# Optimization experiments

Measured on AMD Instinct MI355X. Metric: run time of the kernel, lower is better.

Reference implementation:

```python
import jax, jax.numpy as jnp
import numpy as np

T = 4096        # tokens
D = 1024        # input_dim
H = 2048        # expert_hidden_dim
O = 1024        # output_dim
E = 8           # num_experts
K = 2           # top_k


def setup_inputs() -> dict:
    key = jax.random.key(0)
    ks = jax.random.split(key, 7)
    s_in = 1.0 / np.sqrt(D)
    s_h = 1.0 / np.sqrt(H)
    return {
        "x": jax.random.normal(ks[0], (T, D), dtype=jnp.float32),
        "Wg": jax.random.uniform(ks[1], (D, E), jnp.float32, -s_in, s_in),
        "bg": jax.random.uniform(ks[2], (E,), jnp.float32, -s_in, s_in),
        "W1": jax.random.uniform(ks[3], (E, D, H), jnp.float32, -s_in, s_in),
        "b1": jax.random.uniform(ks[4], (E, H), jnp.float32, -s_in, s_in),
        "W2": jax.random.uniform(ks[5], (E, H, O), jnp.float32, -s_h, s_h),
        "b2": jax.random.uniform(ks[6], (E, O), jnp.float32, -s_h, s_h),
    }


def reference(x, Wg, bg, W1, b1, W2, b2):
    # Gating: top-k over expert logits, softmax over the k selected logits.
    logits = x @ Wg + bg                                  # [T, E]
    top_vals, top_idx = jax.lax.top_k(logits, K)          # [T, K]
    gates = jax.nn.softmax(top_vals, axis=-1)             # [T, K]

    # Expert MLPs (Linear -> ReLU -> Linear). Each token is processed by the
    # experts it routes to; since an expert's output on x is route-independent,
    # compute all expert outputs once and gather the selected ones (static
    # shapes, jit-friendly equivalent of the masked dispatch loop).
    h = jax.nn.relu(jnp.einsum('td,edh->eth', x, W1) + b1[:, None, :])  # [E,T,H]
    y = jnp.einsum('eth,eho->eto', h, W2) + b2[:, None, :]              # [E,T,O]

    sel = y[top_idx, jnp.arange(T)[:, None]]              # [T, K, O]
    # Weighted combine (scatter_add over batch_idx == per-token sum over K).
    return jnp.sum(sel * gates[..., None], axis=1)        # [T, O]
```

## Files before the change

### kernel.cpp

```cpp
#include <hip/hip_runtime.h>
#include <math.h>


#define T_TOK 4096
#define DIM   1024
#define HID   2048
#define OUTD  1024
#define NE    8

typedef __bf16 bf16_t;
typedef __bf16 bf16x8 __attribute__((ext_vector_type(8)));
typedef float  f32x4  __attribute__((ext_vector_type(4)));

typedef __attribute__((address_space(3))) void       as3_void;
typedef __attribute__((address_space(1))) const void as1_void;
#define GLDS16(src, dst) \
  __builtin_amdgcn_global_load_lds((as1_void*)(src), (as3_void*)(dst), 16, 0, 0)

#define FENCE() asm volatile("" ::: "memory")
#define BARRIER() do { FENCE(); __builtin_amdgcn_s_barrier(); FENCE(); } while (0)

__global__ void k_gate(const float* __restrict__ x, const float* __restrict__ Wg,
                       const float* __restrict__ bg, int* __restrict__ einfo,
                       float2* __restrict__ gpair, bf16_t* __restrict__ xb) {
  int wid  = threadIdx.x >> 6;
  int lane = threadIdx.x & 63;
  int t = blockIdx.x * 4 + wid;

  const float4* xr = (const float4*)(x + (size_t)t * DIM);
  float4 xv4[4];
  float sf[NE];
#pragma unroll
  for (int e = 0; e < NE; ++e) sf[e] = 0.f;

#pragma unroll
  for (int i = 0; i < 4; ++i) {
    int q = lane + 64 * i;
    float4 xv = xr[q];
    xv4[i] = xv;
    int d = q * 4;
#pragma unroll
    for (int c = 0; c < 4; ++c) {
      float xc = (&xv.x)[c];
      const float4* wr = (const float4*)(Wg + (size_t)(d + c) * NE);
      float4 w0 = wr[0], w1 = wr[1];
      sf[0] += xc * w0.x; sf[1] += xc * w0.y;
      sf[2] += xc * w0.z; sf[3] += xc * w0.w;
      sf[4] += xc * w1.x; sf[5] += xc * w1.y;
      sf[6] += xc * w1.z; sf[7] += xc * w1.w;
    }
  }

  ushort4* xbr = (ushort4*)(xb + (size_t)t * DIM);
#pragma unroll
  for (int i = 0; i < 4; ++i) {
    union { bf16_t b[4]; ushort4 u; } cv;
    cv.b[0] = (bf16_t)xv4[i].x; cv.b[1] = (bf16_t)xv4[i].y;
    cv.b[2] = (bf16_t)xv4[i].z; cv.b[3] = (bf16_t)xv4[i].w;
    xbr[lane + 64 * i] = cv.u;
  }

  double s[NE];
#pragma unroll
  for (int e = 0; e < NE; ++e) s[e] = (double)sf[e];
#pragma unroll
  for (int off = 32; off > 0; off >>= 1) {
#pragma unroll
    for (int e = 0; e < NE; ++e) s[e] += __shfl_xor(s[e], off);
  }

  if (lane == 0) {
    double v0 = -1e300, v1 = -1e300;
    int i0 = 0, i1 = 0;
#pragma unroll
    for (int e = 0; e < NE; ++e) {
      double v = s[e] + (double)bg[e];
      if (v > v0)      { v1 = v0; i1 = i0; v0 = v; i0 = e; }
      else if (v > v1) { v1 = v;  i1 = e; }
    }
    float ex = expf((float)(v1 - v0));
    float inv = 1.0f / (1.0f + ex);
    einfo[t] = i0 | (i1 << 8);
    gpair[t] = make_float2(inv, ex * inv);
  }
}

__global__ void k_bin(const int* __restrict__ einfo, const float2* __restrict__ gpair,
                      int* __restrict__ cnt, int* __restrict__ offs,
                      int* __restrict__ elist, float* __restrict__ egate,
                      int* __restrict__ tokrec) {
  __shared__ int scnt[NE];
  int w = threadIdx.x >> 6;
  int lane = threadIdx.x & 63;
  unsigned long long below = (lane == 0) ? 0ull : ((~0ull) >> (64 - lane));
  int base = 0;
  for (int c = 0; c < T_TOK / 64; ++c) {
    int t = c * 64 + lane;
    int ei = einfo[t];
    float2 g = gpair[t];
    int e0 = ei & 0xff, e1 = ei >> 8;
    bool m0 = (e0 == w);
    bool m  = m0 || (e1 == w);
    unsigned long long mask = __ballot(m);
    if (m) {
      int pos = base + (int)__popcll(mask & below);
      elist[w * T_TOK + pos] = t;
      egate[w * T_TOK + pos] = m0 ? g.x : g.y;
      tokrec[2 * t + (m0 ? 0 : 1)] = (w << 16) | pos;
    }
    base += (int)__popcll(mask);
  }
  if (lane == 0) scnt[w] = base;
  __syncthreads();
  if (threadIdx.x == 0) {
    int a = 0;
#pragma unroll
    for (int e = 0; e < NE; ++e) {
      cnt[e] = scnt[e];
      offs[e] = a;
      a += scnt[e];
    }
    offs[NE] = a;
  }
}

__global__ void k_tr(const float* __restrict__ W, bf16_t* __restrict__ Wt,
                     int R, int C) {
  __shared__ float tile[32][33];
  size_t ebase = (size_t)blockIdx.z * R * C;
  int c0 = blockIdx.x * 32, r0 = blockIdx.y * 32;
  int id = threadIdx.x;
  int rc = id >> 5, cc = id & 31;
#pragma unroll
  for (int i = 0; i < 4; ++i)
    tile[rc + i * 8][cc] = W[ebase + (size_t)(r0 + rc + i * 8) * C + c0 + cc];
  __syncthreads();
  int oc = id >> 4, orp = id & 15;
  ushort2* wt2 = (ushort2*)(Wt + ebase);
#pragma unroll
  for (int i = 0; i < 2; ++i) {
    int c = oc + i * 16;
    union { bf16_t b[2]; ushort2 u; } cv;
    cv.b[0] = (bf16_t)tile[orp * 2][c];
    cv.b[1] = (bf16_t)tile[orp * 2 + 1][c];
    wt2[((size_t)(c0 + c) * R + r0 + orp * 2) >> 1] = cv.u;
  }
}


#define STAGE_A(TT, HH) do { \
    char* _d = smem + ((((TT) & 1) * 2 + (HH)) << 14); \
    GLDS16(Abase + offA[HH][0] + (TT) * 128, _d + dstq0 * 16); \
    GLDS16(Abase + offA[HH][1] + (TT) * 128, _d + dstq1 * 16); } while (0)

#define STAGE_B(TT, HH) do { \
    char* _d = smem + 65536 + ((((TT) & 1) * 2 + (HH)) << 14); \
    GLDS16(Bbase + offB[HH][0] + (TT) * 128, _d + dstq0 * 16); \
    GLDS16(Bbase + offB[HH][1] + (TT) * 128, _d + dstq1 * 16); } while (0)

#define MFMA_Q(AF, BF, AH, BH) \
    _Pragma("unroll") for (int i = 0; i < 4; ++i) \
      _Pragma("unroll") for (int j = 0; j < 2; ++j) \
        _Pragma("unroll") for (int kk = 0; kk < 2; ++kk) \
          acc[(AH) * 4 + i][(BH) * 2 + j] = \
            __builtin_amdgcn_mfma_f32_16x16x32_bf16(AF[i][kk], BF[j][kk], \
                acc[(AH) * 4 + i][(BH) * 2 + j], 0, 0, 0)

#define LGKM_WAIT() do { \
    asm volatile("s_waitcnt lgkmcnt(0)" ::: "memory"); \
    __builtin_amdgcn_sched_barrier(0); } while (0)

#define KTILE(TT, NTc) do { \
    const char* _a0 = smem + ((((TT) & 1) * 2 + 0) << 14); \
    const char* _a1 = smem + ((((TT) & 1) * 2 + 1) << 14); \
    const char* _b0 = smem + 65536 + ((((TT) & 1) * 2 + 0) << 14); \
    const char* _b1 = smem + 65536 + ((((TT) & 1) * 2 + 1) << 14); \
    bf16x8 af[4][2], bf0[2][2], bf1[2][2]; \
     \
    _Pragma("unroll") for (int i = 0; i < 4; ++i) \
      _Pragma("unroll") for (int kk = 0; kk < 2; ++kk) \
        af[i][kk] = *(const bf16x8*)(_a0 + rdA[i][kk]); \
    _Pragma("unroll") for (int j = 0; j < 2; ++j) \
      _Pragma("unroll") for (int kk = 0; kk < 2; ++kk) { \
        bf0[j][kk] = *(const bf16x8*)(_b0 + rdB[j][kk]); \
        bf1[j][kk] = *(const bf16x8*)(_b1 + rdB[j][kk]); \
      } \
    if ((TT) + 1 < (NTc)) { STAGE_A((TT) + 1, 1); STAGE_B((TT) + 1, 1); } \
    BARRIER(); LGKM_WAIT(); \
    __builtin_amdgcn_s_setprio(1); \
    MFMA_Q(af, bf0, 0, 0); MFMA_Q(af, bf1, 0, 1); \
    __builtin_amdgcn_s_setprio(0); BARRIER(); \
     \
    _Pragma("unroll") for (int i = 0; i < 4; ++i) \
      _Pragma("unroll") for (int kk = 0; kk < 2; ++kk) \
        af[i][kk] = *(const bf16x8*)(_a1 + rdA[i][kk]); \
    if ((TT) + 2 < (NTc)) { STAGE_A((TT) + 2, 0); STAGE_B((TT) + 2, 0); \
      asm volatile("s_waitcnt vmcnt(4)" ::: "memory"); } \
    else { asm volatile("s_waitcnt vmcnt(0)" ::: "memory"); } \
    BARRIER(); LGKM_WAIT(); \
    __builtin_amdgcn_s_setprio(1); \
    MFMA_Q(af, bf0, 1, 0); MFMA_Q(af, bf1, 1, 1); \
    __builtin_amdgcn_s_setprio(0); BARRIER(); \
  } while (0)

__launch_bounds__(512, 2)
__global__ void k_gemm1(const bf16_t* __restrict__ xb, const bf16_t* __restrict__ W1t,
                        const float* __restrict__ b1, const int* __restrict__ cnt,
                        const int* __restrict__ offs, const int* __restrict__ elist,
                        bf16_t* __restrict__ hbuf) {
  const int e = blockIdx.z;
  const int count = cnt[e];
  const int rt = blockIdx.y;
  if (rt * 256 >= count) return;
  const int nt = blockIdx.x;

  __shared__ __align__(16) char smem[131072];

  const int tid = threadIdx.x, lane = tid & 63, wid = tid >> 6;
  const int wm = wid >> 2, wn = wid & 3;
  const int fr = lane & 15, lh = lane >> 4;

  unsigned offA[2][2], offB[2][2];
  const int dstq0 = tid, dstq1 = 512 + tid;
#pragma unroll
  for (int j = 0; j < 2; ++j) {
    int q = j * 512 + tid;
    int r = q >> 3, sfg = (q & 7) ^ (r & 7);
#pragma unroll
    for (int h = 0; h < 2; ++h) {
      int gr = rt * 256 + h * 128 + r;
      if (gr > count - 1) gr = count - 1;
      int tok = elist[e * T_TOK + gr];
      offA[h][j] = (unsigned)((tok * DIM + sfg * 8) * 2);
      int brow = nt * 256 + h * 128 + r;
      offB[h][j] = (unsigned)(((e * HID + brow) * DIM + sfg * 8) * 2);
    }
  }
  unsigned rdA[4][2], rdB[2][2];
#pragma unroll
  for (int i = 0; i < 4; ++i) {
    int r = wm * 64 + i * 16 + fr;
#pragma unroll
    for (int kk = 0; kk < 2; ++kk)
      rdA[i][kk] = (unsigned)(r * 128 + (((kk * 4 + lh) ^ (r & 7)) * 16));
  }
#pragma unroll
  for (int j = 0; j < 2; ++j) {
    int r = wn * 32 + j * 16 + fr;
#pragma unroll
    for (int kk = 0; kk < 2; ++kk)
      rdB[j][kk] = (unsigned)(r * 128 + (((kk * 4 + lh) ^ (r & 7)) * 16));
  }

  const char* Abase = (const char*)xb;
  const char* Bbase = (const char*)W1t;

  f32x4 acc[8][4];
#pragma unroll
  for (int i = 0; i < 8; ++i)
#pragma unroll
    for (int j = 0; j < 4; ++j) acc[i][j] = (f32x4){0.f, 0.f, 0.f, 0.f};

  const int NT = DIM / 64;
  STAGE_A(0, 0); STAGE_B(0, 0); STAGE_A(0, 1); STAGE_B(0, 1);
  STAGE_A(1, 0); STAGE_B(1, 0);
  asm volatile("s_waitcnt vmcnt(4)" ::: "memory");
  BARRIER();

  for (int t = 0; t < NT; ++t) KTILE(t, NT);

  const int hbase = offs[e];
#pragma unroll
  for (int mi = 0; mi < 8; ++mi) {
#pragma unroll
    for (int rr = 0; rr < 4; ++rr) {
      int rowp = rt * 256 + (mi >> 2) * 128 + wm * 64 + (mi & 3) * 16 + lh * 4 + rr;
      if (rowp < count) {
        size_t hrow = (size_t)(hbase + rowp) * HID;
#pragma unroll
        for (int nj = 0; nj < 4; ++nj) {
          int col = nt * 256 + (nj >> 1) * 128 + wn * 32 + (nj & 1) * 16 + fr;
          float v = acc[mi][nj][rr] + b1[e * HID + col];
          hbuf[hrow + col] = (bf16_t)(v > 0.f ? v : 0.f);
        }
      }
    }
  }
}

__launch_bounds__(512, 2)
__global__ void k_gemm2(const bf16_t* __restrict__ hbuf, const bf16_t* __restrict__ W2t,
                        const float* __restrict__ b2, const int* __restrict__ cnt,
                        const int* __restrict__ offs, const float* __restrict__ egate,
                        float* __restrict__ y) {
  const int e = blockIdx.z;
  const int count = cnt[e];
  const int rt = blockIdx.y;
  if (rt * 256 >= count) return;
  const int nt = blockIdx.x;

  __shared__ __align__(16) char smem[131072];

  const int tid = threadIdx.x, lane = tid & 63, wid = tid >> 6;
  const int wm = wid >> 2, wn = wid & 3;
  const int fr = lane & 15, lh = lane >> 4;
  const int hbase = offs[e];

  unsigned offA[2][2], offB[2][2];
  const int dstq0 = tid, dstq1 = 512 + tid;
#pragma unroll
  for (int j = 0; j < 2; ++j) {
    int q = j * 512 + tid;
    int r = q >> 3, sfg = (q & 7) ^ (r & 7);
#pragma unroll
    for (int h = 0; h < 2; ++h) {
      int gr = rt * 256 + h * 128 + r;
      if (gr > count - 1) gr = count - 1;
      offA[h][j] = (unsigned)(((hbase + gr) * HID + sfg * 8) * 2);
      int brow = nt * 256 + h * 128 + r;
      offB[h][j] = (unsigned)(((e * OUTD + brow) * HID + sfg * 8) * 2);
    }
  }
  unsigned rdA[4][2], rdB[2][2];
#pragma unroll
  for (int i = 0; i < 4; ++i) {
    int r = wm * 64 + i * 16 + fr;
#pragma unroll
    for (int kk = 0; kk < 2; ++kk)
      rdA[i][kk] = (unsigned)(r * 128 + (((kk * 4 + lh) ^ (r & 7)) * 16));
  }
#pragma unroll
  for (int j = 0; j < 2; ++j) {
    int r = wn * 32 + j * 16 + fr;
#pragma unroll
    for (int kk = 0; kk < 2; ++kk)
      rdB[j][kk] = (unsigned)(r * 128 + (((kk * 4 + lh) ^ (r & 7)) * 16));
  }

  const char* Abase = (const char*)hbuf;
  const char* Bbase = (const char*)W2t;

  f32x4 acc[8][4];
#pragma unroll
  for (int i = 0; i < 8; ++i)
#pragma unroll
    for (int j = 0; j < 4; ++j) acc[i][j] = (f32x4){0.f, 0.f, 0.f, 0.f};

  const int NT = HID / 64;
  STAGE_A(0, 0); STAGE_B(0, 0); STAGE_A(0, 1); STAGE_B(0, 1);
  STAGE_A(1, 0); STAGE_B(1, 0);
  asm volatile("s_waitcnt vmcnt(4)" ::: "memory");
  BARRIER();

  for (int t = 0; t < NT; ++t) KTILE(t, NT);

#pragma unroll
  for (int mi = 0; mi < 8; ++mi) {
#pragma unroll
    for (int rr = 0; rr < 4; ++rr) {
      int rowp = rt * 256 + (mi >> 2) * 128 + wm * 64 + (mi & 3) * 16 + lh * 4 + rr;
      if (rowp < count) {
        float gate = egate[e * T_TOK + rowp];
        size_t yrow = (size_t)(hbase + rowp) * OUTD;
#pragma unroll
        for (int nj = 0; nj < 4; ++nj) {
          int col = nt * 256 + (nj >> 1) * 128 + wn * 32 + (nj & 1) * 16 + fr;
          y[yrow + col] = gate * (acc[mi][nj][rr] + b2[e * OUTD + col]);
        }
      }
    }
  }
}

__global__ void k_combine(const float* __restrict__ y, const int* __restrict__ offs,
                          const int* __restrict__ tokrec, float* __restrict__ out) {
  int t = blockIdx.x;
  int r0 = tokrec[2 * t], r1 = tokrec[2 * t + 1];
  int s0 = offs[r0 >> 16] + (r0 & 0xffff);
  int s1 = offs[r1 >> 16] + (r1 & 0xffff);
  const float4* ya = (const float4*)(y + (size_t)s0 * OUTD);
  const float4* yb = (const float4*)(y + (size_t)s1 * OUTD);
  float4* o = (float4*)(out + (size_t)t * OUTD);
  int i = threadIdx.x;
  float4 a = ya[i], b = yb[i];
  o[i] = make_float4(a.x + b.x, a.y + b.y, a.z + b.z, a.w + b.w);
}

extern "C" void kernel_launch(void* const* d_in, const int* in_sizes, int n_in,
                              void* d_out, int out_size, void* d_ws, size_t ws_size,
                              hipStream_t stream) {
  const float* x  = (const float*)d_in[0];
  const float* Wg = (const float*)d_in[1];
  const float* bg = (const float*)d_in[2];
  const float* W1 = (const float*)d_in[3];
  const float* b1 = (const float*)d_in[4];
  const float* W2 = (const float*)d_in[5];
  const float* b2 = (const float*)d_in[6];
  float* out = (float*)d_out;

  char* ws = (char*)d_ws;
  int*    cnt    = (int*)(ws);
  int*    offs   = (int*)(ws + 1024);
  int*    tokrec = (int*)(ws + 4096);
  int*    einfo  = (int*)(ws + 36864);
  float2* gpair  = (float2*)(ws + 53248);
  int*    elist  = (int*)(ws + 131072);
  float*  egate  = (float*)(ws + 262144);
  bf16_t* W1t    = (bf16_t*)(ws + (1u << 20));
  float*  y      = (float*)(ws + (1u << 20));
  bf16_t* W2t    = (bf16_t*)(ws + (1u << 20) + (32u << 20));
  bf16_t* xb     = (bf16_t*)(ws + (1u << 20) + (64u << 20));
  bf16_t* hbuf   = (bf16_t*)(ws + (1u << 20) + (72u << 20));

  k_gate<<<T_TOK / 4, 256, 0, stream>>>(x, Wg, bg, einfo, gpair, xb);
  k_bin<<<1, 512, 0, stream>>>(einfo, gpair, cnt, offs, elist, egate, tokrec);
  k_tr<<<dim3(HID / 32, DIM / 32, NE), 256, 0, stream>>>(W1, W1t, DIM, HID);
  k_tr<<<dim3(OUTD / 32, HID / 32, NE), 256, 0, stream>>>(W2, W2t, HID, OUTD);

  k_gemm1<<<dim3(HID / 256, 16, NE), 512, 0, stream>>>(
      xb, W1t, b1, cnt, offs, elist, hbuf);
  k_gemm2<<<dim3(OUTD / 256, 16, NE), 512, 0, stream>>>(
      hbuf, W2t, b2, cnt, offs, egate, y);
  k_combine<<<T_TOK, 256, 0, stream>>>(y, offs, tokrec, out);
}
```

Baseline: 232.4 us.

## Flatten grouped GEMM grid over concatenated expert rows and narrow gemm2 N-tile

Replaces the per-expert 3D grid (which launched mostly empty blocks and padded partial tiles) with a flat grid over the concatenated routed-row space, so each 256-row tile loops over the experts whose segments it overlaps. Tiles that only cover one 128-row half use a dedicated half-tile loop. k_bin now writes a flattened token list for gemm1. gemm2 also shrinks its N tile to 128 to double the block count and cut LDS use to 96KB. In exchange, tiles straddling an expert boundary are computed twice, and the half-tile path synchronises fully on every k-step.

```diff
diff --git a/kernel.cpp b/kernel.cpp
--- a/kernel.cpp
+++ b/kernel.cpp
@@ -19,6 +19,10 @@
 
 #define FENCE() asm volatile("" ::: "memory")
 #define BARRIER() do { FENCE(); __builtin_amdgcn_s_barrier(); FENCE(); } while (0)
+#define LGKM_WAIT() do { \
+    asm volatile("s_waitcnt lgkmcnt(0)" ::: "memory"); \
+    __builtin_amdgcn_sched_barrier(0); } while (0)
+#define VM_WAIT0() asm volatile("s_waitcnt vmcnt(0)" ::: "memory")
 
 __global__ void k_gate(const float* __restrict__ x, const float* __restrict__ Wg,
                        const float* __restrict__ bg, int* __restrict__ einfo,
@@ -88,7 +92,7 @@
 __global__ void k_bin(const int* __restrict__ einfo, const float2* __restrict__ gpair,
                       int* __restrict__ cnt, int* __restrict__ offs,
                       int* __restrict__ elist, float* __restrict__ egate,
-                      int* __restrict__ tokrec) {
+                      int* __restrict__ tokrec, int* __restrict__ ftok) {
   __shared__ int scnt[NE];
   int w = threadIdx.x >> 6;
   int lane = threadIdx.x & 63;
@@ -122,6 +126,13 @@
     }
     offs[NE] = a;
   }
+  int off_w = 0;
+#pragma unroll
+  for (int i = 0; i < NE; ++i)
+    if (i < w) off_w += scnt[i];
+  int n_w = scnt[w];
+  for (int p = lane; p < n_w; p += 64)
+    ftok[off_w + p] = elist[w * T_TOK + p];
 }
 
 __global__ void k_tr(const float* __restrict__ W, bf16_t* __restrict__ Wt,
@@ -147,18 +158,17 @@
   }
 }
 
-
-#define STAGE_A(TT, HH) do { \
+#define STAGE_A1(TT, HH) do { \
     char* _d = smem + ((((TT) & 1) * 2 + (HH)) << 14); \
     GLDS16(Abase + offA[HH][0] + (TT) * 128, _d + dstq0 * 16); \
     GLDS16(Abase + offA[HH][1] + (TT) * 128, _d + dstq1 * 16); } while (0)
 
-#define STAGE_B(TT, HH) do { \
+#define STAGE_B1(TT, HH) do { \
     char* _d = smem + 65536 + ((((TT) & 1) * 2 + (HH)) << 14); \
     GLDS16(Bbase + offB[HH][0] + (TT) * 128, _d + dstq0 * 16); \
     GLDS16(Bbase + offB[HH][1] + (TT) * 128, _d + dstq1 * 16); } while (0)
 
-#define MFMA_Q(AF, BF, AH, BH) \
+#define MFMA_Q1(AF, BF, AH, BH) \
     _Pragma("unroll") for (int i = 0; i < 4; ++i) \
       _Pragma("unroll") for (int j = 0; j < 2; ++j) \
         _Pragma("unroll") for (int kk = 0; kk < 2; ++kk) \
@@ -166,76 +176,90 @@
             __builtin_amdgcn_mfma_f32_16x16x32_bf16(AF[i][kk], BF[j][kk], \
                 acc[(AH) * 4 + i][(BH) * 2 + j], 0, 0, 0)
 
-#define LGKM_WAIT() do { \
-    asm volatile("s_waitcnt lgkmcnt(0)" ::: "memory"); \
-    __builtin_amdgcn_sched_barrier(0); } while (0)
-
-#define KTILE(TT, NTc) do { \
+#define RD_AF1(SL) \
+    _Pragma("unroll") for (int i = 0; i < 4; ++i) \
+      _Pragma("unroll") for (int kk = 0; kk < 2; ++kk) \
+        af[i][kk] = *(const bf16x8*)((SL) + rdA[i][kk])
+
+#define KTILE1(TT, NTc) do { \
     const char* _a0 = smem + ((((TT) & 1) * 2 + 0) << 14); \
     const char* _a1 = smem + ((((TT) & 1) * 2 + 1) << 14); \
     const char* _b0 = smem + 65536 + ((((TT) & 1) * 2 + 0) << 14); \
     const char* _b1 = smem + 65536 + ((((TT) & 1) * 2 + 1) << 14); \
     bf16x8 af[4][2], bf0[2][2], bf1[2][2]; \
-     \
-    _Pragma("unroll") for (int i = 0; i < 4; ++i) \
-      _Pragma("unroll") for (int kk = 0; kk < 2; ++kk) \
-        af[i][kk] = *(const bf16x8*)(_a0 + rdA[i][kk]); \
+    RD_AF1(_a0); \
     _Pragma("unroll") for (int j = 0; j < 2; ++j) \
       _Pragma("unroll") for (int kk = 0; kk < 2; ++kk) { \
         bf0[j][kk] = *(const bf16x8*)(_b0 + rdB[j][kk]); \
         bf1[j][kk] = *(const bf16x8*)(_b1 + rdB[j][kk]); \
       } \
-    if ((TT) + 1 < (NTc)) { STAGE_A((TT) + 1, 1); STAGE_B((TT) + 1, 1); } \
+    if ((TT) + 1 < (NTc)) { STAGE_A1((TT) + 1, 1); STAGE_B1((TT) + 1, 1); } \
     BARRIER(); LGKM_WAIT(); \
     __builtin_amdgcn_s_setprio(1); \
-    MFMA_Q(af, bf0, 0, 0); MFMA_Q(af, bf1, 0, 1); \
+    MFMA_Q1(af, bf0, 0, 0); MFMA_Q1(af, bf1, 0, 1); \
     __builtin_amdgcn_s_setprio(0); BARRIER(); \
-     \
-    _Pragma("unroll") for (int i = 0; i < 4; ++i) \
-      _Pragma("unroll") for (int kk = 0; kk < 2; ++kk) \
-        af[i][kk] = *(const bf16x8*)(_a1 + rdA[i][kk]); \
-    if ((TT) + 2 < (NTc)) { STAGE_A((TT) + 2, 0); STAGE_B((TT) + 2, 0); \
+    RD_AF1(_a1); \
+    if ((TT) + 2 < (NTc)) { STAGE_A1((TT) + 2, 0); STAGE_B1((TT) + 2, 0); \
       asm volatile("s_waitcnt vmcnt(4)" ::: "memory"); } \
-    else { asm volatile("s_waitcnt vmcnt(0)" ::: "memory"); } \
+    else { VM_WAIT0(); } \
     BARRIER(); LGKM_WAIT(); \
     __builtin_amdgcn_s_setprio(1); \
-    MFMA_Q(af, bf0, 1, 0); MFMA_Q(af, bf1, 1, 1); \
+    MFMA_Q1(af, bf0, 1, 0); MFMA_Q1(af, bf1, 1, 1); \
     __builtin_amdgcn_s_setprio(0); BARRIER(); \
   } while (0)
 
+#define G1_HALF(H) do { \
+    STAGE_A1(0, H); STAGE_B1(0, 0); STAGE_B1(0, 1); \
+    VM_WAIT0(); BARRIER(); \
+    for (int t = 0; t < NT; ++t) { \
+      const char* _a  = smem + (((t & 1) * 2 + (H)) << 14); \
+      const char* _b0 = smem + 65536 + (((t & 1) * 2 + 0) << 14); \
+      const char* _b1 = smem + 65536 + (((t & 1) * 2 + 1) << 14); \
+      bf16x8 af[4][2], bf0[2][2], bf1[2][2]; \
+      RD_AF1(_a); \
+      _Pragma("unroll") for (int j = 0; j < 2; ++j) \
+        _Pragma("unroll") for (int kk = 0; kk < 2; ++kk) { \
+          bf0[j][kk] = *(const bf16x8*)(_b0 + rdB[j][kk]); \
+          bf1[j][kk] = *(const bf16x8*)(_b1 + rdB[j][kk]); \
+        } \
+      if (t + 1 < NT) { STAGE_A1(t + 1, H); STAGE_B1(t + 1, 0); STAGE_B1(t + 1, 1); } \
+      LGKM_WAIT(); \
+      __builtin_amdgcn_s_setprio(1); \
+      MFMA_Q1(af, bf0, H, 0); MFMA_Q1(af, bf1, H, 1); \
+      __builtin_amdgcn_s_setprio(0); \
+      VM_WAIT0(); BARRIER(); \
+    } \
+  } while (0)
+
 __launch_bounds__(512, 2)
 __global__ void k_gemm1(const bf16_t* __restrict__ xb, const bf16_t* __restrict__ W1t,
-                        const float* __restrict__ b1, const int* __restrict__ cnt,
-                        const int* __restrict__ offs, const int* __restrict__ elist,
-                        bf16_t* __restrict__ hbuf) {
-  const int e = blockIdx.z;
-  const int count = cnt[e];
-  const int rt = blockIdx.y;
-  if (rt * 256 >= count) return;
-  const int nt = blockIdx.x;
+                        const float* __restrict__ b1, const int* __restrict__ offs,
+                        const int* __restrict__ ftok, bf16_t* __restrict__ hbuf) {
+  const int bid = blockIdx.x;
+  const int nt = bid & 7, rt = bid >> 3;
+  const int r0 = rt * 256;
 
   __shared__ __align__(16) char smem[131072];
 
   const int tid = threadIdx.x, lane = tid & 63, wid = tid >> 6;
   const int wm = wid >> 2, wn = wid & 3;
   const int fr = lane & 15, lh = lane >> 4;
-
-  unsigned offA[2][2], offB[2][2];
   const int dstq0 = tid, dstq1 = 512 + tid;
+
+  int rowq[2], sfgq[2];
 #pragma unroll
   for (int j = 0; j < 2; ++j) {
     int q = j * 512 + tid;
-    int r = q >> 3, sfg = (q & 7) ^ (r & 7);
-#pragma unroll
-    for (int h = 0; h < 2; ++h) {
-      int gr = rt * 256 + h * 128 + r;
-      if (gr > count - 1) gr = count - 1;
-      int tok = elist[e * T_TOK + gr];
-      offA[h][j] = (unsigned)((tok * DIM + sfg * 8) * 2);
-      int brow = nt * 256 + h * 128 + r;
-      offB[h][j] = (unsigned)(((e * HID + brow) * DIM + sfg * 8) * 2);
-    }
-  }
+    rowq[j] = q >> 3;
+    sfgq[j] = (q & 7) ^ (rowq[j] & 7);
+  }
+  unsigned offA[2][2];
+#pragma unroll
+  for (int j = 0; j < 2; ++j)
+#pragma unroll
+    for (int h = 0; h < 2; ++h)
+      offA[h][j] = (unsigned)((ftok[r0 + h * 128 + rowq[j]] * DIM + sfgq[j] * 8) * 2);
+
   unsigned rdA[4][2], rdB[2][2];
 #pragma unroll
   for (int i = 0; i < 4; ++i) {
@@ -254,74 +278,165 @@
 
   const char* Abase = (const char*)xb;
   const char* Bbase = (const char*)W1t;
-
-  f32x4 acc[8][4];
-#pragma unroll
-  for (int i = 0; i < 8; ++i)
-#pragma unroll
-    for (int j = 0; j < 4; ++j) acc[i][j] = (f32x4){0.f, 0.f, 0.f, 0.f};
-
   const int NT = DIM / 64;
-  STAGE_A(0, 0); STAGE_B(0, 0); STAGE_A(0, 1); STAGE_B(0, 1);
-  STAGE_A(1, 0); STAGE_B(1, 0);
-  asm volatile("s_waitcnt vmcnt(4)" ::: "memory");
-  BARRIER();
-
-  for (int t = 0; t < NT; ++t) KTILE(t, NT);
-
-  const int hbase = offs[e];
-#pragma unroll
-  for (int mi = 0; mi < 8; ++mi) {
-#pragma unroll
-    for (int rr = 0; rr < 4; ++rr) {
-      int rowp = rt * 256 + (mi >> 2) * 128 + wm * 64 + (mi & 3) * 16 + lh * 4 + rr;
-      if (rowp < count) {
-        size_t hrow = (size_t)(hbase + rowp) * HID;
-#pragma unroll
-        for (int nj = 0; nj < 4; ++nj) {
-          int col = nt * 256 + (nj >> 1) * 128 + wn * 32 + (nj & 1) * 16 + fr;
-          float v = acc[mi][nj][rr] + b1[e * HID + col];
-          hbuf[hrow + col] = (bf16_t)(v > 0.f ? v : 0.f);
+
+  int e = 0;
+  while (offs[e + 1] <= r0) ++e;
+  for (;;) {
+    const int lo = offs[e] > r0 ? offs[e] : r0;
+    const int hi = offs[e + 1] < r0 + 256 ? offs[e + 1] : r0 + 256;
+    if (hi > lo) {
+      unsigned offB[2][2];
+#pragma unroll
+      for (int j = 0; j < 2; ++j)
+#pragma unroll
+        for (int h = 0; h < 2; ++h)
+          offB[h][j] = (unsigned)(((e * HID + nt * 256 + h * 128 + rowq[j]) * DIM +
+                                   sfgq[j] * 8) * 2);
+
+      f32x4 acc[8][4];
+#pragma unroll
+      for (int i = 0; i < 8; ++i)
+#pragma unroll
+        for (int j = 0; j < 4; ++j) acc[i][j] = (f32x4){0.f, 0.f, 0.f, 0.f};
+
+      const bool fh0 = lo < r0 + 128, fh1 = hi > r0 + 128;
+      if (fh0 && fh1) {
+        STAGE_A1(0, 0); STAGE_B1(0, 0); STAGE_A1(0, 1); STAGE_B1(0, 1);
+        STAGE_A1(1, 0); STAGE_B1(1, 0);
+        asm volatile("s_waitcnt vmcnt(4)" ::: "memory");
+        BARRIER();
+        for (int t = 0; t < NT; ++t) KTILE1(t, NT);
+      } else if (fh0) {
+        G1_HALF(0);
+      } else {
+        G1_HALF(1);
+      }
+
+#pragma unroll
+      for (int mi = 0; mi < 8; ++mi) {
+#pragma unroll
+        for (int rr = 0; rr < 4; ++rr) {
+          int row = r0 + (mi >> 2) * 128 + wm * 64 + (mi & 3) * 16 + lh * 4 + rr;
+          if (row >= lo && row < hi) {
+            size_t hrow = (size_t)row * HID;
+#pragma unroll
+            for (int nj = 0; nj < 4; ++nj) {
+              int col = nt * 256 + (nj >> 1) * 128 + wn * 32 + (nj & 1) * 16 + fr;
+              float v = acc[mi][nj][rr] + b1[e * HID + col];
+              hbuf[hrow + col] = (bf16_t)(v > 0.f ? v : 0.f);
+            }
+          }
         }
       }
     }
-  }
-}
+    if (offs[e + 1] >= r0 + 256) break;
+    ++e;
+  }
+}
+
+#define STAGE_A2(TT, HH) do { \
+    char* _d = smem + ((((TT) & 1) * 2 + (HH)) << 14); \
+    GLDS16(Abase + offA[HH][0] + (TT) * 128, _d + dstq0 * 16); \
+    GLDS16(Abase + offA[HH][1] + (TT) * 128, _d + dstq1 * 16); } while (0)
+
+#define STAGE_B2(TT, HH) do { \
+    char* _d = smem + 65536 + ((((TT) & 1) * 2 + (HH)) << 13); \
+    GLDS16(Bbase + offB2[HH] + (TT) * 128, _d + tid * 16); } while (0)
+
+#define MFMA_Q2(AF, BF, AH, BH) \
+    _Pragma("unroll") for (int i = 0; i < 4; ++i) \
+      _Pragma("unroll") for (int kk = 0; kk < 2; ++kk) \
+        acc[(AH) * 4 + i][BH] = \
+          __builtin_amdgcn_mfma_f32_16x16x32_bf16(AF[i][kk], BF[kk], \
+              acc[(AH) * 4 + i][BH], 0, 0, 0)
+
+#define RD_AF2(SL) \
+    _Pragma("unroll") for (int i = 0; i < 4; ++i) \
+      _Pragma("unroll") for (int kk = 0; kk < 2; ++kk) \
+        af[i][kk] = *(const bf16x8*)((SL) + rdA[i][kk])
+
+#define KTILE2(TT, NTc) do { \
+    const char* _a0 = smem + ((((TT) & 1) * 2 + 0) << 14); \
+    const char* _a1 = smem + ((((TT) & 1) * 2 + 1) << 14); \
+    const char* _b0 = smem + 65536 + ((((TT) & 1) * 2 + 0) << 13); \
+    const char* _b1 = smem + 65536 + ((((TT) & 1) * 2 + 1) << 13); \
+    bf16x8 af[4][2], bf0[2], bf1[2]; \
+    RD_AF2(_a0); \
+    _Pragma("unroll") for (int kk = 0; kk < 2; ++kk) { \
+      bf0[kk] = *(const bf16x8*)(_b0 + rdB2[kk]); \
+      bf1[kk] = *(const bf16x8*)(_b1 + rdB2[kk]); \
+    } \
+    if ((TT) + 1 < (NTc)) { STAGE_A2((TT) + 1, 1); STAGE_B2((TT) + 1, 1); } \
+    BARRIER(); LGKM_WAIT(); \
+    __builtin_amdgcn_s_setprio(1); \
+    MFMA_Q2(af, bf0, 0, 0); MFMA_Q2(af, bf1, 0, 1); \
+    __builtin_amdgcn_s_setprio(0); BARRIER(); \
+    RD_AF2(_a1); \
+    if ((TT) + 2 < (NTc)) { STAGE_A2((TT) + 2, 0); STAGE_B2((TT) + 2, 0); \
+      asm volatile("s_waitcnt vmcnt(3)" ::: "memory"); } \
+    else { VM_WAIT0(); } \
+    BARRIER(); LGKM_WAIT(); \
+    __builtin_amdgcn_s_setprio(1); \
+    MFMA_Q2(af, bf0, 1, 0); MFMA_Q2(af, bf1, 1, 1); \
+    __builtin_amdgcn_s_setprio(0); BARRIER(); \
+  } while (0)
+
+#define G2_HALF(H) do { \
+    STAGE_A2(0, H); STAGE_B2(0, 0); STAGE_B2(0, 1); \
+    VM_WAIT0(); BARRIER(); \
+    for (int t = 0; t < NT; ++t) { \
+      const char* _a  = smem + (((t & 1) * 2 + (H)) << 14); \
+      const char* _b0 = smem + 65536 + (((t & 1) * 2 + 0) << 13); \
+      const char* _b1 = smem + 65536 + (((t & 1) * 2 + 1) << 13); \
+      bf16x8 af[4][2], bf0[2], bf1[2]; \
+      RD_AF2(_a); \
+      _Pragma("unroll") for (int kk = 0; kk < 2; ++kk) { \
+        bf0[kk] = *(const bf16x8*)(_b0 + rdB2[kk]); \
+        bf1[kk] = *(const bf16x8*)(_b1 + rdB2[kk]); \
+      } \
+      if (t + 1 < NT) { STAGE_A2(t + 1, H); STAGE_B2(t + 1, 0); STAGE_B2(t + 1, 1); } \
+      LGKM_WAIT(); \
+      __builtin_amdgcn_s_setprio(1); \
+      MFMA_Q2(af, bf0, H, 0); MFMA_Q2(af, bf1, H, 1); \
+      __builtin_amdgcn_s_setprio(0); \
+      VM_WAIT0(); BARRIER(); \
+    } \
+  } while (0)
 
 __launch_bounds__(512, 2)
 __global__ void k_gemm2(const bf16_t* __restrict__ hbuf, const bf16_t* __restrict__ W2t,
-                        const float* __restrict__ b2, const int* __restrict__ cnt,
-                        const int* __restrict__ offs, const float* __restrict__ egate,
-                        float* __restrict__ y) {
-  const int e = blockIdx.z;
-  const int count = cnt[e];
-  const int rt = blockIdx.y;
-  if (rt * 256 >= count) return;
-  const int nt = blockIdx.x;
-
-  __shared__ __align__(16) char smem[131072];
+                        const float* __restrict__ b2, const int* __restrict__ offs,
+                        const float* __restrict__ egate, float* __restrict__ y) {
+  const int bid = blockIdx.x;
+  const int nt = bid & 7, rt = bid >> 3;
+  const int r0 = rt * 256;
+
+  __shared__ __align__(16) char smem[98304];
 
   const int tid = threadIdx.x, lane = tid & 63, wid = tid >> 6;
   const int wm = wid >> 2, wn = wid & 3;
   const int fr = lane & 15, lh = lane >> 4;
-  const int hbase = offs[e];
-
-  unsigned offA[2][2], offB[2][2];
   const int dstq0 = tid, dstq1 = 512 + tid;
+
+  int rowq[2], sfgq[2];
 #pragma unroll
   for (int j = 0; j < 2; ++j) {
     int q = j * 512 + tid;
-    int r = q >> 3, sfg = (q & 7) ^ (r & 7);
-#pragma unroll
-    for (int h = 0; h < 2; ++h) {
-      int gr = rt * 256 + h * 128 + r;
-      if (gr > count - 1) gr = count - 1;
-      offA[h][j] = (unsigned)(((hbase + gr) * HID + sfg * 8) * 2);
-      int brow = nt * 256 + h * 128 + r;
-      offB[h][j] = (unsigned)(((e * OUTD + brow) * HID + sfg * 8) * 2);
-    }
-  }
-  unsigned rdA[4][2], rdB[2][2];
+    rowq[j] = q >> 3;
+    sfgq[j] = (q & 7) ^ (rowq[j] & 7);
+  }
+  unsigned offA[2][2];
+#pragma unroll
+  for (int j = 0; j < 2; ++j)
+#pragma unroll
+    for (int h = 0; h < 2; ++h)
+      offA[h][j] = (unsigned)(((r0 + h * 128 + rowq[j]) * HID + sfgq[j] * 8) * 2);
+
+  const int rowB = tid >> 3;
+  const int sfgB = (tid & 7) ^ (rowB & 7);
+
+  unsigned rdA[4][2], rdB2[2];
 #pragma unroll
   for (int i = 0; i < 4; ++i) {
     int r = wm * 64 + i * 16 + fr;
@@ -329,46 +444,67 @@
     for (int kk = 0; kk < 2; ++kk)
       rdA[i][kk] = (unsigned)(r * 128 + (((kk * 4 + lh) ^ (r & 7)) * 16));
   }
-#pragma unroll
-  for (int j = 0; j < 2; ++j) {
-    int r = wn * 32 + j * 16 + fr;
+  {
+    int r = wn * 16 + fr;
 #pragma unroll
     for (int kk = 0; kk < 2; ++kk)
-      rdB[j][kk] = (unsigned)(r * 128 + (((kk * 4 + lh) ^ (r & 7)) * 16));
+      rdB2[kk] = (unsigned)(r * 128 + (((kk * 4 + lh) ^ (r & 7)) * 16));
   }
 
   const char* Abase = (const char*)hbuf;
   const char* Bbase = (const char*)W2t;
-
-  f32x4 acc[8][4];
-#pragma unroll
-  for (int i = 0; i < 8; ++i)
-#pragma unroll
-    for (int j = 0; j < 4; ++j) acc[i][j] = (f32x4){0.f, 0.f, 0.f, 0.f};
-
   const int NT = HID / 64;
-  STAGE_A(0, 0); STAGE_B(0, 0); STAGE_A(0, 1); STAGE_B(0, 1);
-  STAGE_A(1, 0); STAGE_B(1, 0);
-  asm volatile("s_waitcnt vmcnt(4)" ::: "memory");
-  BARRIER();
-
-  for (int t = 0; t < NT; ++t) KTILE(t, NT);
-
-#pragma unroll
-  for (int mi = 0; mi < 8; ++mi) {
-#pragma unroll
-    for (int rr = 0; rr < 4; ++rr) {
-      int rowp = rt * 256 + (mi >> 2) * 128 + wm * 64 + (mi & 3) * 16 + lh * 4 + rr;
-      if (rowp < count) {
-        float gate = egate[e * T_TOK + rowp];
-        size_t yrow = (size_t)(hbase + rowp) * OUTD;
-#pragma unroll
-        for (int nj = 0; nj < 4; ++nj) {
-          int col = nt * 256 + (nj >> 1) * 128 + wn * 32 + (nj & 1) * 16 + fr;
-          y[yrow + col] = gate * (acc[mi][nj][rr] + b2[e * OUTD + col]);
+
+  int e = 0;
+  while (offs[e + 1] <= r0) ++e;
+  for (;;) {
+    const int lo = offs[e] > r0 ? offs[e] : r0;
+    const int hi = offs[e + 1] < r0 + 256 ? offs[e + 1] : r0 + 256;
+    if (hi > lo) {
+      unsigned offB2[2];
+#pragma unroll
+      for (int h = 0; h < 2; ++h)
+        offB2[h] = (unsigned)(((e * OUTD + nt * 128 + h * 64 + rowB) * HID +
+                               sfgB * 8) * 2);
+
+      f32x4 acc[8][2];
+#pragma unroll
+      for (int i = 0; i < 8; ++i)
+#pragma unroll
+        for (int j = 0; j < 2; ++j) acc[i][j] = (f32x4){0.f, 0.f, 0.f, 0.f};
+
+      const bool fh0 = lo < r0 + 128, fh1 = hi > r0 + 128;
+      if (fh0 && fh1) {
+        STAGE_A2(0, 0); STAGE_B2(0, 0); STAGE_A2(0, 1); STAGE_B2(0, 1);
+        STAGE_A2(1, 0); STAGE_B2(1, 0);
+        asm volatile("s_waitcnt vmcnt(3)" ::: "memory");
+        BARRIER();
+        for (int t = 0; t < NT; ++t) KTILE2(t, NT);
+      } else if (fh0) {
+        G2_HALF(0);
+      } else {
+        G2_HALF(1);
+      }
+
+#pragma unroll
+      for (int mi = 0; mi < 8; ++mi) {
+#pragma unroll
+        for (int rr = 0; rr < 4; ++rr) {
+          int row = r0 + (mi >> 2) * 128 + wm * 64 + (mi & 3) * 16 + lh * 4 + rr;
+          if (row >= lo && row < hi) {
+            float gate = egate[e * T_TOK + row - offs[e]];
+            size_t yrow = (size_t)row * OUTD;
+#pragma unroll
+            for (int bh = 0; bh < 2; ++bh) {
+              int col = nt * 128 + bh * 64 + wn * 16 + fr;
+              y[yrow + col] = gate * (acc[mi][bh][rr] + b2[e * OUTD + col]);
+            }
+          }
         }
       }
     }
+    if (offs[e + 1] >= r0 + 256) break;
+    ++e;
   }
 }
 
@@ -406,6 +542,7 @@
   float2* gpair  = (float2*)(ws + 53248);
   int*    elist  = (int*)(ws + 131072);
   float*  egate  = (float*)(ws + 262144);
+  int*    ftok   = (int*)(ws + 393216);
   bf16_t* W1t    = (bf16_t*)(ws + (1u << 20));
   float*  y      = (float*)(ws + (1u << 20));
   bf16_t* W2t    = (bf16_t*)(ws + (1u << 20) + (32u << 20));
@@ -413,13 +550,13 @@
   bf16_t* hbuf   = (bf16_t*)(ws + (1u << 20) + (72u << 20));
 
   k_gate<<<T_TOK / 4, 256, 0, stream>>>(x, Wg, bg, einfo, gpair, xb);
-  k_bin<<<1, 512, 0, stream>>>(einfo, gpair, cnt, offs, elist, egate, tokrec);
+  k_bin<<<1, 512, 0, stream>>>(einfo, gpair, cnt, offs, elist, egate, tokrec, ftok);
   k_tr<<<dim3(HID / 32, DIM / 32, NE), 256, 0, stream>>>(W1, W1t, DIM, HID);
   k_tr<<<dim3(OUTD / 32, HID / 32, NE), 256, 0, stream>>>(W2, W2t, HID, OUTD);
 
-  k_gemm1<<<dim3(HID / 256, 16, NE), 512, 0, stream>>>(
-      xb, W1t, b1, cnt, offs, elist, hbuf);
-  k_gemm2<<<dim3(OUTD / 256, 16, NE), 512, 0, stream>>>(
-      hbuf, W2t, b2, cnt, offs, egate, y);
+  k_gemm1<<<(T_TOK * 2 / 256) * (HID / 256), 512, 0, stream>>>(
+      xb, W1t, b1, offs, ftok, hbuf);
+  k_gemm2<<<(T_TOK * 2 / 256) * (OUTD / 128), 512, 0, stream>>>(
+      hbuf, W2t, b2, offs, egate, y);
   k_combine<<<T_TOK, 256, 0, stream>>>(y, offs, tokrec, out);
 }
```

Measured after the change: 304.3 us. 31.0% more time.

## Shrink GEMM M-tile to 192 rows and vectorize weight transpose

Applied to the files above, without the earlier changes.

The expert GEMMs now use 192-row token tiles instead of 256. This changes the LDS staging layout, the per-wave accumulator count, and the per-wave vmcnt waits, since some waves issue fewer async loads. The grid grows to 22 row tiles. The goal is to cut padded-row waste on per-expert token counts and improve load balance, at the cost of less reuse of each B tile. The weight transpose kernel switches to 64x64 tiles with float4 loads and 16-byte bf16 stores to reduce memory transactions.

```diff
diff --git a/kernel.cpp b/kernel.cpp
--- a/kernel.cpp
+++ b/kernel.cpp
@@ -19,6 +19,13 @@
 
 #define FENCE() asm volatile("" ::: "memory")
 #define BARRIER() do { FENCE(); __builtin_amdgcn_s_barrier(); FENCE(); } while (0)
+#define LGKM_WAIT() do { \
+    asm volatile("s_waitcnt lgkmcnt(0)" ::: "memory"); \
+    __builtin_amdgcn_sched_barrier(0); } while (0)
+#define VMW_RING() do { \
+    if (wid < 4) asm volatile("s_waitcnt vmcnt(4)" ::: "memory"); \
+    else         asm volatile("s_waitcnt vmcnt(3)" ::: "memory"); } while (0)
+#define VM_WAIT0() asm volatile("s_waitcnt vmcnt(0)" ::: "memory")
 
 __global__ void k_gate(const float* __restrict__ x, const float* __restrict__ Wg,
                        const float* __restrict__ bg, int* __restrict__ einfo,
@@ -126,60 +133,61 @@
 
 __global__ void k_tr(const float* __restrict__ W, bf16_t* __restrict__ Wt,
                      int R, int C) {
-  __shared__ float tile[32][33];
+  __shared__ float tile[64][68];
   size_t ebase = (size_t)blockIdx.z * R * C;
-  int c0 = blockIdx.x * 32, r0 = blockIdx.y * 32;
-  int id = threadIdx.x;
-  int rc = id >> 5, cc = id & 31;
-#pragma unroll
-  for (int i = 0; i < 4; ++i)
-    tile[rc + i * 8][cc] = W[ebase + (size_t)(r0 + rc + i * 8) * C + c0 + cc];
+  int c0 = blockIdx.x * 64, r0 = blockIdx.y * 64;
+  int tid = threadIdx.x;
+  int ty = tid >> 4, tx = tid & 15;
+#pragma unroll
+  for (int i = 0; i < 4; ++i) {
+    int row = ty + i * 16;
+    float4 v = *(const float4*)&W[ebase + (size_t)(r0 + row) * C + c0 + tx * 4];
+    *(float4*)&tile[row][tx * 4] = v;
+  }
   __syncthreads();
-  int oc = id >> 4, orp = id & 15;
-  ushort2* wt2 = (ushort2*)(Wt + ebase);
-#pragma unroll
-  for (int i = 0; i < 2; ++i) {
-    int c = oc + i * 16;
-    union { bf16_t b[2]; ushort2 u; } cv;
-    cv.b[0] = (bf16_t)tile[orp * 2][c];
-    cv.b[1] = (bf16_t)tile[orp * 2 + 1][c];
-    wt2[((size_t)(c0 + c) * R + r0 + orp * 2) >> 1] = cv.u;
-  }
-}
-
+  int oc = tid >> 2, seg = tid & 3;
+#pragma unroll
+  for (int half = 0; half < 2; ++half) {
+    union { bf16_t b[8]; uint4 u; } cv;
+#pragma unroll
+    for (int r = 0; r < 8; ++r)
+      cv.b[r] = (bf16_t)tile[seg * 16 + half * 8 + r][oc];
+    *(uint4*)&Wt[ebase + (size_t)(c0 + oc) * R + r0 + seg * 16 + half * 8] = cv.u;
+  }
+}
 
 #define STAGE_A(TT, HH) do { \
-    char* _d = smem + ((((TT) & 1) * 2 + (HH)) << 14); \
-    GLDS16(Abase + offA[HH][0] + (TT) * 128, _d + dstq0 * 16); \
-    GLDS16(Abase + offA[HH][1] + (TT) * 128, _d + dstq1 * 16); } while (0)
+    char* _d = smem + (((TT) & 1) * 24576) + ((HH) * 12288); \
+    GLDS16(Abase + offA[HH][0] + (TT) * 128, _d + tid * 16); \
+    if (tid < 256) GLDS16(Abase + offA[HH][1] + (TT) * 128, _d + (512 + tid) * 16); \
+  } while (0)
 
 #define STAGE_B(TT, HH) do { \
-    char* _d = smem + 65536 + ((((TT) & 1) * 2 + (HH)) << 14); \
-    GLDS16(Bbase + offB[HH][0] + (TT) * 128, _d + dstq0 * 16); \
-    GLDS16(Bbase + offB[HH][1] + (TT) * 128, _d + dstq1 * 16); } while (0)
+    char* _d = smem + 49152 + (((TT) & 1) * 32768) + ((HH) * 16384); \
+    GLDS16(Bbase + offB[HH][0] + (TT) * 128, _d + tid * 16); \
+    GLDS16(Bbase + offB[HH][1] + (TT) * 128, _d + (512 + tid) * 16); \
+  } while (0)
 
 #define MFMA_Q(AF, BF, AH, BH) \
-    _Pragma("unroll") for (int i = 0; i < 4; ++i) \
+    _Pragma("unroll") for (int i = 0; i < 3; ++i) \
       _Pragma("unroll") for (int j = 0; j < 2; ++j) \
         _Pragma("unroll") for (int kk = 0; kk < 2; ++kk) \
-          acc[(AH) * 4 + i][(BH) * 2 + j] = \
+          acc[(AH) * 3 + i][(BH) * 2 + j] = \
             __builtin_amdgcn_mfma_f32_16x16x32_bf16(AF[i][kk], BF[j][kk], \
-                acc[(AH) * 4 + i][(BH) * 2 + j], 0, 0, 0)
-
-#define LGKM_WAIT() do { \
-    asm volatile("s_waitcnt lgkmcnt(0)" ::: "memory"); \
-    __builtin_amdgcn_sched_barrier(0); } while (0)
+                acc[(AH) * 3 + i][(BH) * 2 + j], 0, 0, 0)
+
+#define RD_AF(SL) \
+    _Pragma("unroll") for (int i = 0; i < 3; ++i) \
+      _Pragma("unroll") for (int kk = 0; kk < 2; ++kk) \
+        af[i][kk] = *(const bf16x8*)((SL) + rdA[i][kk])
 
 #define KTILE(TT, NTc) do { \
-    const char* _a0 = smem + ((((TT) & 1) * 2 + 0) << 14); \
-    const char* _a1 = smem + ((((TT) & 1) * 2 + 1) << 14); \
-    const char* _b0 = smem + 65536 + ((((TT) & 1) * 2 + 0) << 14); \
-    const char* _b1 = smem + 65536 + ((((TT) & 1) * 2 + 1) << 14); \
-    bf16x8 af[4][2], bf0[2][2], bf1[2][2]; \
-     \
-    _Pragma("unroll") for (int i = 0; i < 4; ++i) \
-      _Pragma("unroll") for (int kk = 0; kk < 2; ++kk) \
-        af[i][kk] = *(const bf16x8*)(_a0 + rdA[i][kk]); \
+    const char* _a0 = smem + (((TT) & 1) * 24576); \
+    const char* _a1 = smem + (((TT) & 1) * 24576) + 12288; \
+    const char* _b0 = smem + 49152 + (((TT) & 1) * 32768); \
+    const char* _b1 = smem + 49152 + (((TT) & 1) * 32768) + 16384; \
+    bf16x8 af[3][2], bf0[2][2], bf1[2][2]; \
+    RD_AF(_a0); \
     _Pragma("unroll") for (int j = 0; j < 2; ++j) \
       _Pragma("unroll") for (int kk = 0; kk < 2; ++kk) { \
         bf0[j][kk] = *(const bf16x8*)(_b0 + rdB[j][kk]); \
@@ -190,13 +198,10 @@
     __builtin_amdgcn_s_setprio(1); \
     MFMA_Q(af, bf0, 0, 0); MFMA_Q(af, bf1, 0, 1); \
     __builtin_amdgcn_s_setprio(0); BARRIER(); \
-     \
-    _Pragma("unroll") for (int i = 0; i < 4; ++i) \
-      _Pragma("unroll") for (int kk = 0; kk < 2; ++kk) \
-        af[i][kk] = *(const bf16x8*)(_a1 + rdA[i][kk]); \
+    RD_AF(_a1); \
     if ((TT) + 2 < (NTc)) { STAGE_A((TT) + 2, 0); STAGE_B((TT) + 2, 0); \
-      asm volatile("s_waitcnt vmcnt(4)" ::: "memory"); } \
-    else { asm volatile("s_waitcnt vmcnt(0)" ::: "memory"); } \
+      VMW_RING(); } \
+    else { VM_WAIT0(); } \
     BARRIER(); LGKM_WAIT(); \
     __builtin_amdgcn_s_setprio(1); \
     MFMA_Q(af, bf0, 1, 0); MFMA_Q(af, bf1, 1, 1); \
@@ -211,24 +216,23 @@
   const int e = blockIdx.z;
   const int count = cnt[e];
   const int rt = blockIdx.y;
-  if (rt * 256 >= count) return;
+  if (rt * 192 >= count) return;
   const int nt = blockIdx.x;
 
-  __shared__ __align__(16) char smem[131072];
+  __shared__ __align__(16) char smem[114688];
 
   const int tid = threadIdx.x, lane = tid & 63, wid = tid >> 6;
   const int wm = wid >> 2, wn = wid & 3;
   const int fr = lane & 15, lh = lane >> 4;
 
   unsigned offA[2][2], offB[2][2];
-  const int dstq0 = tid, dstq1 = 512 + tid;
 #pragma unroll
   for (int j = 0; j < 2; ++j) {
     int q = j * 512 + tid;
     int r = q >> 3, sfg = (q & 7) ^ (r & 7);
 #pragma unroll
     for (int h = 0; h < 2; ++h) {
-      int gr = rt * 256 + h * 128 + r;
+      int gr = rt * 192 + h * 96 + r;
       if (gr > count - 1) gr = count - 1;
       int tok = elist[e * T_TOK + gr];
       offA[h][j] = (unsigned)((tok * DIM + sfg * 8) * 2);
@@ -236,10 +240,10 @@
       offB[h][j] = (unsigned)(((e * HID + brow) * DIM + sfg * 8) * 2);
     }
   }
-  unsigned rdA[4][2], rdB[2][2];
-#pragma unroll
-  for (int i = 0; i < 4; ++i) {
-    int r = wm * 64 + i * 16 + fr;
+  unsigned rdA[3][2], rdB[2][2];
+#pragma unroll
+  for (int i = 0; i < 3; ++i) {
+    int r = wm * 48 + i * 16 + fr;
 #pragma unroll
     for (int kk = 0; kk < 2; ++kk)
       rdA[i][kk] = (unsigned)(r * 128 + (((kk * 4 + lh) ^ (r & 7)) * 16));
@@ -255,26 +259,26 @@
   const char* Abase = (const char*)xb;
   const char* Bbase = (const char*)W1t;
 
-  f32x4 acc[8][4];
-#pragma unroll
-  for (int i = 0; i < 8; ++i)
+  f32x4 acc[6][4];
+#pragma unroll
+  for (int i = 0; i < 6; ++i)
 #pragma unroll
     for (int j = 0; j < 4; ++j) acc[i][j] = (f32x4){0.f, 0.f, 0.f, 0.f};
 
   const int NT = DIM / 64;
   STAGE_A(0, 0); STAGE_B(0, 0); STAGE_A(0, 1); STAGE_B(0, 1);
   STAGE_A(1, 0); STAGE_B(1, 0);
-  asm volatile("s_waitcnt vmcnt(4)" ::: "memory");
+  VMW_RING();
   BARRIER();
 
   for (int t = 0; t < NT; ++t) KTILE(t, NT);
 
   const int hbase = offs[e];
 #pragma unroll
-  for (int mi = 0; mi < 8; ++mi) {
+  for (int mi = 0; mi < 6; ++mi) {
 #pragma unroll
     for (int rr = 0; rr < 4; ++rr) {
-      int rowp = rt * 256 + (mi >> 2) * 128 + wm * 64 + (mi & 3) * 16 + lh * 4 + rr;
+      int rowp = rt * 192 + (mi / 3) * 96 + wm * 48 + (mi % 3) * 16 + lh * 4 + rr;
       if (rowp < count) {
         size_t hrow = (size_t)(hbase + rowp) * HID;
 #pragma unroll
@@ -296,10 +300,10 @@
   const int e = blockIdx.z;
   const int count = cnt[e];
   const int rt = blockIdx.y;
-  if (rt * 256 >= count) return;
+  if (rt * 192 >= count) return;
   const int nt = blockIdx.x;
 
-  __shared__ __align__(16) char smem[131072];
+  __shared__ __align__(16) char smem[114688];
 
   const int tid = threadIdx.x, lane = tid & 63, wid = tid >> 6;
   const int wm = wid >> 2, wn = wid & 3;
@@ -307,24 +311,23 @@
   const int hbase = offs[e];
 
   unsigned offA[2][2], offB[2][2];
-  const int dstq0 = tid, dstq1 = 512 + tid;
 #pragma unroll
   for (int j = 0; j < 2; ++j) {
     int q = j * 512 + tid;
     int r = q >> 3, sfg = (q & 7) ^ (r & 7);
 #pragma unroll
     for (int h = 0; h < 2; ++h) {
-      int gr = rt * 256 + h * 128 + r;
+      int gr = rt * 192 + h * 96 + r;
       if (gr > count - 1) gr = count - 1;
       offA[h][j] = (unsigned)(((hbase + gr) * HID + sfg * 8) * 2);
       int brow = nt * 256 + h * 128 + r;
       offB[h][j] = (unsigned)(((e * OUTD + brow) * HID + sfg * 8) * 2);
     }
   }
-  unsigned rdA[4][2], rdB[2][2];
-#pragma unroll
-  for (int i = 0; i < 4; ++i) {
-    int r = wm * 64 + i * 16 + fr;
+  unsigned rdA[3][2], rdB[2][2];
+#pragma unroll
+  for (int i = 0; i < 3; ++i) {
+    int r = wm * 48 + i * 16 + fr;
 #pragma unroll
     for (int kk = 0; kk < 2; ++kk)
       rdA[i][kk] = (unsigned)(r * 128 + (((kk * 4 + lh) ^ (r & 7)) * 16));
@@ -340,25 +343,25 @@
   const char* Abase = (const char*)hbuf;
   const char* Bbase = (const char*)W2t;
 
-  f32x4 acc[8][4];
-#pragma unroll
-  for (int i = 0; i < 8; ++i)
+  f32x4 acc[6][4];
+#pragma unroll
+  for (int i = 0; i < 6; ++i)
 #pragma unroll
     for (int j = 0; j < 4; ++j) acc[i][j] = (f32x4){0.f, 0.f, 0.f, 0.f};
 
   const int NT = HID / 64;
   STAGE_A(0, 0); STAGE_B(0, 0); STAGE_A(0, 1); STAGE_B(0, 1);
   STAGE_A(1, 0); STAGE_B(1, 0);
-  asm volatile("s_waitcnt vmcnt(4)" ::: "memory");
+  VMW_RING();
   BARRIER();
 
   for (int t = 0; t < NT; ++t) KTILE(t, NT);
 
 #pragma unroll
-  for (int mi = 0; mi < 8; ++mi) {
+  for (int mi = 0; mi < 6; ++mi) {
 #pragma unroll
     for (int rr = 0; rr < 4; ++rr) {
-      int rowp = rt * 256 + (mi >> 2) * 128 + wm * 64 + (mi & 3) * 16 + lh * 4 + rr;
+      int rowp = rt * 192 + (mi / 3) * 96 + wm * 48 + (mi % 3) * 16 + lh * 4 + rr;
       if (rowp < count) {
         float gate = egate[e * T_TOK + rowp];
         size_t yrow = (size_t)(hbase + rowp) * OUTD;
@@ -414,12 +417,12 @@
 
   k_gate<<<T_TOK / 4, 256, 0, stream>>>(x, Wg, bg, einfo, gpair, xb);
   k_bin<<<1, 512, 0, stream>>>(einfo, gpair, cnt, offs, elist, egate, tokrec);
-  k_tr<<<dim3(HID / 32, DIM / 32, NE), 256, 0, stream>>>(W1, W1t, DIM, HID);
-  k_tr<<<dim3(OUTD / 32, HID / 32, NE), 256, 0, stream>>>(W2, W2t, HID, OUTD);
-
-  k_gemm1<<<dim3(HID / 256, 16, NE), 512, 0, stream>>>(
+  k_tr<<<dim3(HID / 64, DIM / 64, NE), 256, 0, stream>>>(W1, W1t, DIM, HID);
+  k_tr<<<dim3(OUTD / 64, HID / 64, NE), 256, 0, stream>>>(W2, W2t, HID, OUTD);
+
+  k_gemm1<<<dim3(HID / 256, 22, NE), 512, 0, stream>>>(
       xb, W1t, b1, cnt, offs, elist, hbuf);
-  k_gemm2<<<dim3(OUTD / 256, 16, NE), 512, 0, stream>>>(
+  k_gemm2<<<dim3(OUTD / 256, 22, NE), 512, 0, stream>>>(
       hbuf, W2t, b2, cnt, offs, egate, y);
   k_combine<<<T_TOK, 256, 0, stream>>>(y, offs, tokrec, out);
 }
```

Result: faster. 208.9 us (-10.1%).
